# Kernel optimization log

Measured on AMD Instinct MI355X. Metric: run time of the kernel, lower is better.

The kernel has to match this reference:

```python
import jax, jax.numpy as jnp
import numpy as np

BATCH = 32768
DIM = 256
NUM_LATENTS = 4096
ENTROPY_WEIGHT = 0.1
VQ_BETA = 0.25
EPS = 1e-9


def _l2_normalize(v, axis=-1, eps=1e-12):
    # matches torch F.normalize(dim=-1)
    n = jnp.linalg.norm(v, axis=axis, keepdims=True)
    return v / jnp.maximum(n, eps)


def setup_inputs() -> dict:
    key = jax.random.key(0)
    kx, kc = jax.random.split(key)
    x = jax.random.normal(kx, (BATCH, DIM), dtype=jnp.float32)
    # codebook initialized uniform(-bound, bound) then row-normalized, as in __init__
    bound = (3.0 / DIM) ** 0.5
    cb = jax.random.uniform(kc, (NUM_LATENTS, DIM), dtype=jnp.float32,
                            minval=-bound, maxval=bound)
    codebook = _l2_normalize(cb)
    return {"x": x, "codebook": codebook}


def reference(x, codebook):
    # cosine-distance nearest-code lookup
    x_norm = _l2_normalize(x)                       # [B, D]
    cb_norm = _l2_normalize(codebook)               # [K, D]
    distance = -jnp.einsum('bd,kd->bk', x_norm, cb_norm)  # [B, K]
    # dropout p=0.0 -> identity
    indices = jnp.argmin(distance, axis=-1)         # [B] int
    z = codebook[indices]                           # [B, D] gather

    # straight-through estimator
    z_q = x + jax.lax.stop_gradient(z - x)

    commit_loss = jnp.mean((x - jax.lax.stop_gradient(z)) ** 2)
    q_loss = jnp.mean((z - jax.lax.stop_gradient(x)) ** 2)

    # entropy of codebook usage
    counts = jnp.bincount(indices, length=NUM_LATENTS).astype(jnp.float32)
    probs = counts / counts.sum()
    entropy = -jnp.sum(probs * jnp.log(jnp.clip(probs, EPS)))
    entropy_loss = -entropy

    vq_loss = q_loss + VQ_BETA * commit_loss + ENTROPY_WEIGHT * entropy_loss
    return (z_q, vq_loss, q_loss, commit_loss, entropy_loss, entropy, indices)
```

## Files before the change

kernel.cpp:

```cpp
#include <hip/hip_runtime.h>
#include <math.h>

#define BATCH 32768
#define DIM   256
#define NLAT  4096

typedef _Float16 f16x8 __attribute__((ext_vector_type(8)));
typedef float    f32x16 __attribute__((ext_vector_type(16)));

#define WS_CBH    0u
#define WS_CBINV  2097152u
#define WS_KEYS   2113536u
#define WS_HIST   4210688u

__device__ inline float kdec(uint key) {
  return __uint_as_float(key & 0xFFFFF000u);
}

__global__ __launch_bounds__(256) void prep_kernel(
    const float* __restrict__ x, const float* __restrict__ cb,
    ushort* __restrict__ cbhf, float* __restrict__ cbinv,
    ushort* __restrict__ xhf, int* __restrict__ hist) {
  int bid = blockIdx.x;
  if (bid < 1024) {
    int w = threadIdx.x >> 6, l = threadIdx.x & 63;
    int row = bid * 4 + w;
    const float4* cr = (const float4*)(cb + (size_t)row * DIM);
    float4 v = cr[l];
    float s = v.x * v.x + v.y * v.y + v.z * v.z + v.w * v.w;
    #pragma unroll
    for (int m = 32; m; m >>= 1) s += __shfl_xor(s, m, 64);
    float inv = 1.0f / fmaxf(sqrtf(s), 1e-12f);
    if (l == 0) cbinv[row] = inv;
    union { _Float16 h[4]; uint2 u; } pk;
    pk.h[0] = (_Float16)(v.x * inv);
    pk.h[1] = (_Float16)(v.y * inv);
    pk.h[2] = (_Float16)(v.z * inv);
    pk.h[3] = (_Float16)(v.w * inv);
    int t  = row >> 6, rf = (row >> 5) & 1, l31r = row & 31;
    int sl = l >> 2, lh2 = (l >> 1) & 1, half = l & 1;
    int lane = lh2 * 32 + l31r;
    ((uint2*)cbhf)[(((t * 16 + sl) * 2 + rf) << 7) + lane * 2 + half] = pk.u;
  } else if (bid < 5120) {
    int idx = (bid - 1024) * 256 + threadIdx.x;
    const float4* xs = (const float4*)x;
    float4 a = xs[idx * 2];
    float4 b = xs[idx * 2 + 1];
    union { _Float16 h[8]; uint4 u; } pk;
    pk.h[0] = (_Float16)a.x; pk.h[1] = (_Float16)a.y;
    pk.h[2] = (_Float16)a.z; pk.h[3] = (_Float16)a.w;
    pk.h[4] = (_Float16)b.x; pk.h[5] = (_Float16)b.y;
    pk.h[6] = (_Float16)b.z; pk.h[7] = (_Float16)b.w;
    int row = idx >> 5, c = idx & 31;
    int rowgrp = row >> 5, l31r = row & 31, sl = c >> 1, lhh = c & 1;
    ((uint4*)xhf)[((size_t)rowgrp * 16 + sl) * 64 + lhh * 32 + l31r] = pk.u;
  } else {
    for (int k = threadIdx.x; k < NLAT; k += 256) hist[k] = 0;
  }
}

__global__ __launch_bounds__(256, 4) void vq_gemm_kernel(
    const char* __restrict__ xhf, const char* __restrict__ cbhf,
    uint* __restrict__ keys) {
  const int tid = threadIdx.x;
  const int w = tid >> 6, l = tid & 63;
  const int l31 = l & 31, lh = l >> 5;
  const int bb = blockIdx.x >> 2, q = blockIdx.x & 3;
  const int wrow0 = bb * 128 + w * 32;
  const int cbase = q * 1024;
  const uint lh4u = (uint)(lh << 2);

  const char* xb = xhf + ((size_t)(bb * 4 + w) * 1024 + l) * 16;
  f16x8 xf[16];
  #pragma unroll
  for (int s2 = 0; s2 < 16; ++s2) xf[s2] = *(const f16x8*)(xb + s2 * 1024);

  const char* qbase = cbhf + (size_t)q * 524288 + (size_t)l * 16;
  f16x8 ring[2][2];
  ring[0][0] = *(const f16x8*)(qbase);
  ring[0][1] = *(const f16x8*)(qbase + 1024);
  const char* pp = qbase + 2048;

  uint k1 = 0, k2 = 0, k3 = 0;

  #pragma unroll 1
  for (int t = 0; t < 16; ++t) {
    f32x16 acc[2];
    #pragma unroll
    for (int r = 0; r < 16; ++r) { acc[0][r] = 32.0f; acc[1][r] = 32.0f; }

    #pragma unroll
    for (int sl = 0; sl < 16; ++sl) {
      ring[(sl + 1) & 1][0] = *(const f16x8*)(pp);
      ring[(sl + 1) & 1][1] = *(const f16x8*)(pp + 1024);
      pp += 2048;
      acc[0] = __builtin_amdgcn_mfma_f32_32x32x16_f16(
          ring[sl & 1][0], xf[sl], acc[0], 0, 0, 0);
      acc[1] = __builtin_amdgcn_mfma_f32_32x32x16_f16(
          ring[sl & 1][1], xf[sl], acc[1], 0, 0, 0);
    }

    const uint scode = (uint)(cbase + t * 64);
    #pragma unroll
    for (int rf = 0; rf < 2; ++rf) {
      #pragma unroll
      for (int r = 0; r < 16; ++r) {
        const uint cr = (uint)(rf * 32 + (r & 3) + 8 * (r >> 2));
        uint key = (__float_as_uint(acc[rf][r]) & 0xFFFFF000u)
                 | scode | cr | lh4u;
        uint m1 = max(k1, key), n1 = min(k1, key); k1 = m1;
        uint m2 = max(k2, n1),  n2 = min(k2, n1);  k2 = m2;
        k3 = max(k3, n2);
      }
    }
  }

  uint o1 = __shfl_xor(k1, 32, 64);
  uint o2 = __shfl_xor(k2, 32, 64);
  uint o3 = __shfl_xor(k3, 32, 64);
  uint k4 = 0;
  #pragma unroll
  for (int e = 0; e < 3; ++e) {
    uint o = (e == 0) ? o1 : (e == 1) ? o2 : o3;
    uint m = max(k1, o), n = min(k1, o); k1 = m;
    m = max(k2, n); n = min(k2, n); k2 = m;
    m = max(k3, n); n = min(k3, n); k3 = m;
    k4 = max(k4, n);
  }
  if (lh == 0) {
    uint4 kv; kv.x = k1; kv.y = k2; kv.z = k3; kv.w = k4;
    *(uint4*)(keys + (size_t)(wrow0 + l31) * 16 + q * 4) = kv;
  }
}

__global__ __launch_bounds__(256) void rescore_kernel(
    const float* __restrict__ x, const float* __restrict__ cb,
    const float* __restrict__ cbinv, const uint* __restrict__ keys,
    float* __restrict__ zq, float* __restrict__ out_idx,
    int* __restrict__ hist, double* __restrict__ psse) {
  __shared__ float part[4];
  int tid = threadIdx.x, w = tid >> 6, l = tid & 63;
  int row = blockIdx.x * 4 + w;
  const float4* xr = (const float4*)(x + (size_t)row * DIM);
  float4 xv = xr[l];
  float s0 = xv.x * xv.x + xv.y * xv.y + xv.z * xv.z + xv.w * xv.w;
  #pragma unroll
  for (int m = 32; m; m >>= 1) s0 += __shfl_xor(s0, m, 64);
  float xnorm = sqrtf(s0);
  float xinv = 1.0f / fmaxf(xnorm, 1e-12f);

  uint key = keys[row * 16 + (l & 15)];
  uint kmax = key;
  #pragma unroll
  for (int m = 1; m < 16; m <<= 1) {
    uint o = __shfl_xor(kmax, m, 64);
    kmax = (o > kmax) ? o : kmax;
  }
  float dmax = kdec(kmax);
  float thr = dmax - 2.0f * (3e-3f * xnorm);
  bool inwin = (kdec(key) >= thr) && (l < 16);
  unsigned long long mask = __ballot(inwin);
  int besti;
  if (__popcll(mask) == 1) {
    besti = (int)(kmax & 0xFFFu);
  } else {
    float bestv = -3e38f; besti = 0x7fffffff;
    unsigned long long mm = mask;
    while (mm) {
      int b = __ffsll(mm) - 1; mm &= mm - 1;
      int ci = (int)(__shfl(key, b, 64) & 0xFFFu);
      float cbi = cbinv[ci];
      const float4* cr = (const float4*)(cb + (size_t)ci * DIM);
      float4 cv = cr[l];
      float d = (xv.x * xinv) * (cv.x * cbi) + (xv.y * xinv) * (cv.y * cbi)
              + (xv.z * xinv) * (cv.z * cbi) + (xv.w * xinv) * (cv.w * cbi);
      #pragma unroll
      for (int m = 32; m; m >>= 1) d += __shfl_xor(d, m, 64);
      bool better = (d > bestv) || (d == bestv && ci < besti);
      bestv = better ? d : bestv;
      besti = better ? ci : besti;
    }
  }

  float4 zv = ((const float4*)(cb + (size_t)besti * DIM))[l];
  float4 o;
  o.x = xv.x + (zv.x - xv.x); o.y = xv.y + (zv.y - xv.y);
  o.z = xv.z + (zv.z - xv.z); o.w = xv.w + (zv.w - xv.w);
  ((float4*)(zq + (size_t)row * DIM))[l] = o;
  float dx = xv.x - zv.x, dy = xv.y - zv.y, dz = xv.z - zv.z, dw = xv.w - zv.w;
  float s = dx * dx + dy * dy + dz * dz + dw * dw;
  #pragma unroll
  for (int m = 32; m; m >>= 1) s += __shfl_xor(s, m, 64);
  if (l == 0) part[w] = s;
  __syncthreads();
  if (tid == 0)
    psse[blockIdx.x] = (double)((part[0] + part[1]) + (part[2] + part[3]));
  if (l == 0) {
    atomicAdd(&hist[besti], 1);
    out_idx[row] = (float)besti;
  }
}

__global__ __launch_bounds__(256) void finalize_kernel(
    const int* __restrict__ hist, const double* __restrict__ psse,
    float* __restrict__ outs) {
  int tid = threadIdx.x;
  double e = 0.0, s = 0.0;
  for (int k = tid; k < NLAT; k += 256) {
    int c = hist[k];
    if (c > 0) {
      float p = (float)c * (1.0f / 32768.0f);
      e += (double)(p * logf(p));
    }
  }
  for (int k = tid; k < BATCH / 4; k += 256) s += psse[k];
  #pragma unroll
  for (int off = 32; off; off >>= 1) {
    e += __shfl_xor(e, off, 64);
    s += __shfl_xor(s, off, 64);
  }
  __shared__ double pe[4], ps[4];
  int w = tid >> 6, l = tid & 63;
  if (l == 0) { pe[w] = e; ps[w] = s; }
  __syncthreads();
  if (tid == 0) {
    double H = -((pe[0] + pe[1]) + (pe[2] + pe[3]));
    double sse = (ps[0] + ps[1]) + (ps[2] + ps[3]);
    double qv = sse * (1.0 / ((double)BATCH * (double)DIM));
    float qf = (float)qv;
    float Hf = (float)H;
    float ent_loss = -Hf;
    float vq = qf + 0.25f * qf + 0.1f * ent_loss;
    outs[0] = vq;
    outs[1] = qf;
    outs[2] = qf;
    outs[3] = ent_loss;
    outs[4] = Hf;
  }
}

extern "C" void kernel_launch(void* const* d_in, const int* in_sizes, int n_in,
                              void* d_out, int out_size, void* d_ws, size_t ws_size,
                              hipStream_t stream) {
  const float* x  = (const float*)d_in[0];
  const float* cb = (const float*)d_in[1];

  float* out     = (float*)d_out;
  float* zq      = out;
  float* scalars = out + (size_t)BATCH * DIM;
  float* oidx    = scalars + 5;

  char* wsb = (char*)d_ws;
  ushort* cbhf  = (ushort*)(wsb + WS_CBH);
  float*  cbinv = (float*)(wsb + WS_CBINV);
  uint*   keys  = (uint*)(wsb + WS_KEYS);
  int*    hist  = (int*)(wsb + WS_HIST);
  double* psse  = (double*)(wsb + WS_CBH);

  ushort* xhf = (ushort*)d_out;

  prep_kernel<<<5121, 256, 0, stream>>>(x, cb, cbhf, cbinv, xhf, hist);
  vq_gemm_kernel<<<1024, 256, 0, stream>>>((const char*)xhf,
                                           (const char*)cbhf, keys);
  rescore_kernel<<<BATCH / 4, 256, 0, stream>>>(x, cb, cbinv, keys,
                                                zq, oidx, hist, psse);
  finalize_kernel<<<1, 256, 0, stream>>>(hist, psse, scalars);
}
```

Baseline: 222.3 us.

## Split prep into norm and pack kernels, deepen GEMM prefetch ring with barrier/priority

The prep step is split into two kernels. One computes codebook inverse norms and clears the histogram. The other packs the codebook and x into the fp16 MFMA layout, with each thread writing one contiguous 16-byte output, so the stores are coalesced and the scattered writes go away. In the GEMM, the codebook register ring grows from 2 to 4 stages with a prefetch distance of 2, and each tile is wrapped in a workgroup barrier, with raised wave priority around the MFMAs. This adds one kernel launch, a re-read of the codebook, higher register pressure and a per-tile barrier that could stall waves.

```diff
diff --git a/kernel.cpp b/kernel.cpp
--- a/kernel.cpp
+++ b/kernel.cpp
@@ -17,10 +17,9 @@
   return __uint_as_float(key & 0xFFFFF000u);
 }
 
-__global__ __launch_bounds__(256) void prep_kernel(
-    const float* __restrict__ x, const float* __restrict__ cb,
-    ushort* __restrict__ cbhf, float* __restrict__ cbinv,
-    ushort* __restrict__ xhf, int* __restrict__ hist) {
+__global__ __launch_bounds__(256) void prep1_kernel(
+    const float* __restrict__ cb, float* __restrict__ cbinv,
+    int* __restrict__ hist) {
   int bid = blockIdx.x;
   if (bid < 1024) {
     int w = threadIdx.x >> 6, l = threadIdx.x & 63;
@@ -30,32 +29,48 @@
     float s = v.x * v.x + v.y * v.y + v.z * v.z + v.w * v.w;
     #pragma unroll
     for (int m = 32; m; m >>= 1) s += __shfl_xor(s, m, 64);
-    float inv = 1.0f / fmaxf(sqrtf(s), 1e-12f);
-    if (l == 0) cbinv[row] = inv;
-    union { _Float16 h[4]; uint2 u; } pk;
-    pk.h[0] = (_Float16)(v.x * inv);
-    pk.h[1] = (_Float16)(v.y * inv);
-    pk.h[2] = (_Float16)(v.z * inv);
-    pk.h[3] = (_Float16)(v.w * inv);
-    int t  = row >> 6, rf = (row >> 5) & 1, l31r = row & 31;
-    int sl = l >> 2, lh2 = (l >> 1) & 1, half = l & 1;
-    int lane = lh2 * 32 + l31r;
-    ((uint2*)cbhf)[(((t * 16 + sl) * 2 + rf) << 7) + lane * 2 + half] = pk.u;
-  } else if (bid < 5120) {
-    int idx = (bid - 1024) * 256 + threadIdx.x;
+    if (l == 0) cbinv[row] = 1.0f / fmaxf(sqrtf(s), 1e-12f);
+  } else {
+    for (int k = threadIdx.x; k < NLAT; k += 256) hist[k] = 0;
+  }
+}
+
+__global__ __launch_bounds__(256) void prep2_kernel(
+    const float* __restrict__ x, const float* __restrict__ cb,
+    const float* __restrict__ cbinv, uint4* __restrict__ cbhf4,
+    uint4* __restrict__ xhf4) {
+  int bid = blockIdx.x, tid = threadIdx.x;
+  if (bid < 512) {
+    int gid = bid * 256 + tid;
+    int frag = gid >> 6, lane = gid & 63;
+    int rf = frag & 1, ts = frag >> 1, sl = ts & 15, t = ts >> 4;
+    int row = t * 64 + rf * 32 + (lane & 31);
+    int e4 = sl * 4 + (lane >> 5) * 2;
+    const float4* cr = (const float4*)(cb + (size_t)row * DIM);
+    float inv = cbinv[row];
+    float4 a = cr[e4], b = cr[e4 + 1];
+    union { _Float16 h[8]; uint4 u; } pk;
+    pk.h[0] = (_Float16)(a.x * inv); pk.h[1] = (_Float16)(a.y * inv);
+    pk.h[2] = (_Float16)(a.z * inv); pk.h[3] = (_Float16)(a.w * inv);
+    pk.h[4] = (_Float16)(b.x * inv); pk.h[5] = (_Float16)(b.y * inv);
+    pk.h[6] = (_Float16)(b.z * inv); pk.h[7] = (_Float16)(b.w * inv);
+    cbhf4[gid] = pk.u;
+  } else {
+    int o = (bid - 512) * 256 + tid;
+    int rowgrp = o >> 10, rem = o & 1023;
+    int sl = rem >> 6, rem2 = rem & 63;
+    int lhh = rem2 >> 5, l31r = rem2 & 31;
+    int row = rowgrp * 32 + l31r;
+    int c = sl * 2 + lhh;
     const float4* xs = (const float4*)x;
-    float4 a = xs[idx * 2];
-    float4 b = xs[idx * 2 + 1];
+    float4 a = xs[(size_t)row * 64 + c * 2];
+    float4 b = xs[(size_t)row * 64 + c * 2 + 1];
     union { _Float16 h[8]; uint4 u; } pk;
     pk.h[0] = (_Float16)a.x; pk.h[1] = (_Float16)a.y;
     pk.h[2] = (_Float16)a.z; pk.h[3] = (_Float16)a.w;
     pk.h[4] = (_Float16)b.x; pk.h[5] = (_Float16)b.y;
     pk.h[6] = (_Float16)b.z; pk.h[7] = (_Float16)b.w;
-    int row = idx >> 5, c = idx & 31;
-    int rowgrp = row >> 5, l31r = row & 31, sl = c >> 1, lhh = c & 1;
-    ((uint4*)xhf)[((size_t)rowgrp * 16 + sl) * 64 + lhh * 32 + l31r] = pk.u;
-  } else {
-    for (int k = threadIdx.x; k < NLAT; k += 256) hist[k] = 0;
+    xhf4[o] = pk.u;
   }
 }
 
@@ -76,28 +91,34 @@
   for (int s2 = 0; s2 < 16; ++s2) xf[s2] = *(const f16x8*)(xb + s2 * 1024);
 
   const char* qbase = cbhf + (size_t)q * 524288 + (size_t)l * 16;
-  f16x8 ring[2][2];
-  ring[0][0] = *(const f16x8*)(qbase);
-  ring[0][1] = *(const f16x8*)(qbase + 1024);
-  const char* pp = qbase + 2048;
+  f16x8 ring[4][2];
+  #pragma unroll
+  for (int s = 0; s < 2; ++s) {
+    ring[s][0] = *(const f16x8*)(qbase + s * 2048);
+    ring[s][1] = *(const f16x8*)(qbase + s * 2048 + 1024);
+  }
+  const char* pp = qbase + 4096;
 
   uint k1 = 0, k2 = 0, k3 = 0;
 
   #pragma unroll 1
   for (int t = 0; t < 16; ++t) {
+    __builtin_amdgcn_s_barrier();
     f32x16 acc[2];
     #pragma unroll
     for (int r = 0; r < 16; ++r) { acc[0][r] = 32.0f; acc[1][r] = 32.0f; }
 
     #pragma unroll
     for (int sl = 0; sl < 16; ++sl) {
-      ring[(sl + 1) & 1][0] = *(const f16x8*)(pp);
-      ring[(sl + 1) & 1][1] = *(const f16x8*)(pp + 1024);
+      ring[(sl + 2) & 3][0] = *(const f16x8*)(pp);
+      ring[(sl + 2) & 3][1] = *(const f16x8*)(pp + 1024);
       pp += 2048;
+      __builtin_amdgcn_s_setprio(1);
       acc[0] = __builtin_amdgcn_mfma_f32_32x32x16_f16(
-          ring[sl & 1][0], xf[sl], acc[0], 0, 0, 0);
+          ring[sl & 3][0], xf[sl], acc[0], 0, 0, 0);
       acc[1] = __builtin_amdgcn_mfma_f32_32x32x16_f16(
-          ring[sl & 1][1], xf[sl], acc[1], 0, 0, 0);
+          ring[sl & 3][1], xf[sl], acc[1], 0, 0, 0);
+      __builtin_amdgcn_s_setprio(0);
     }
 
     const uint scode = (uint)(cbase + t * 64);
@@ -259,7 +280,9 @@
 
   ushort* xhf = (ushort*)d_out;
 
-  prep_kernel<<<5121, 256, 0, stream>>>(x, cb, cbhf, cbinv, xhf, hist);
+  prep1_kernel<<<1025, 256, 0, stream>>>(cb, cbinv, hist);
+  prep2_kernel<<<4608, 256, 0, stream>>>(x, cb, cbinv,
+                                         (uint4*)cbhf, (uint4*)xhf);
   vq_gemm_kernel<<<1024, 256, 0, stream>>>((const char*)xhf,
                                            (const char*)cbhf, keys);
   rescore_kernel<<<BATCH / 4, 256, 0, stream>>>(x, cb, cbinv, keys,
```

New measurement: 232.2 us. 1.04x slower.
